# Optimization experiments

Hardware: AMD Instinct MI355X
Metric: run time of the kernel (lower is better)

The kernel has to match this reference:

```python
import jax, jax.numpy as jnp
import numpy as np

N, E, D = 50000, 800000, 64


def setup_inputs() -> dict:
    key = jax.random.key(0)
    k = jax.random.split(key, 6)
    return {
        "graph_embedding": jax.random.normal(k[0], (N, D), dtype=jnp.float32),
        "W": jax.random.normal(k[1], (D, D), dtype=jnp.float32) * (1.0 / np.sqrt(D)),
        "b": jnp.zeros((D,), dtype=jnp.float32),
        "src": jax.random.randint(k[2], (E,), 0, N),
        "dst": jax.random.randint(k[3], (E,), 0, N),
        "e_feat": jax.random.randint(k[4], (E,), 0, 8),
    }


def _gcn_both(x, src, dst, n, W=None, b=None):
    # DGL GraphConv with norm='both': D_out^{-1/2} gather-sum D_in^{-1/2}, then optional weight.
    ones = jnp.ones((src.shape[0],), x.dtype)
    out_deg = jnp.maximum(jax.ops.segment_sum(ones, src, num_segments=n), 1.0)
    in_deg = jnp.maximum(jax.ops.segment_sum(ones, dst, num_segments=n), 1.0)
    x = x * (out_deg ** -0.5)[:, None]
    agg = jax.ops.segment_sum(x[src], dst, num_segments=n)  # [N, D]
    agg = agg * (in_deg ** -0.5)[:, None]
    if W is not None:
        agg = agg @ W + b
    return agg


def reference(graph_embedding, W, b, src, dst, e_feat):
    n = graph_embedding.shape[0]
    # dropout is identity in eval mode
    h = _gcn_both(graph_embedding, src, dst, n)       # layer 0: weight=False
    h = _gcn_both(h, src, dst, n, W, b)               # layer 1: with weight + bias
    # message: ft + sum of masked copies; all ft0/ft2/ft4/ft6 == ft, so per-edge scale
    e = e_feat.reshape(-1, 1).astype(jnp.float32)     # [E, 1], mirrors e_feat.reshape(-1,1).float()
    coef = (1.0 + (e == 0.0) + (e == 2.0) + (e == 4.0) + (e == 6.0)).astype(h.dtype)
    msg = h[src] * coef                               # [E, D] edge gather + scale
    return jax.ops.segment_sum(msg, dst, num_segments=n)  # scatter-sum to dst
```

## Files before the change

### kernel.cpp

```cpp
#include <hip/hip_runtime.h>

#define DD 64
#define CHUNK_A 4096

__global__ __launch_bounds__(256) void k_pre(const int* __restrict__ src,
                                             const int* __restrict__ dst,
                                             int* __restrict__ M,
                                             int* __restrict__ cout_, int E, int PB) {
    int t = threadIdx.x;
    int bid = blockIdx.x;
    if (bid < PB) {
        __shared__ int hist[256];
        hist[t] = 0;
        __syncthreads();
        int base = bid * CHUNK_A;
#pragma unroll
        for (int k = 0; k < CHUNK_A / 256; ++k) {
            int e = base + t + (k << 8);
            if (e < E) atomicAdd(&hist[dst[e] >> 8], 1);
        }
        __syncthreads();
        M[bid * 256 + t] = hist[t];
    } else {
        int e = (bid - PB) * 256 + t;
        if (e < E) atomicAdd(&cout_[src[e]], 1);
    }
}

__global__ __launch_bounds__(256) void k_binscan(int* __restrict__ M,
                                                 int* __restrict__ binBase,
                                                 int* __restrict__ rstart,
                                                 const int* __restrict__ cout_,
                                                 float* __restrict__ oinv,
                                                 int PB, int n, int E) {
    int t = threadIdx.x;
    if (blockIdx.x == 0) {
        int tot = 0;
        for (int p = 0; p < PB; ++p) tot += M[p * 256 + t];
        int lane = t & 63, w = t >> 6;
        int inc = tot;
        for (int o = 1; o < 64; o <<= 1) {
            int u = __shfl_up(inc, o);
            if (lane >= o) inc += u;
        }
        __shared__ int wtot[4];
        if (lane == 63) wtot[w] = inc;
        __syncthreads();
        int woff = 0;
        for (int i = 0; i < w; ++i) woff += wtot[i];
        int base = woff + inc - tot;
        binBase[t] = base;
        if (t == 255) { binBase[256] = base + tot; rstart[n] = E; }
        int run = base;
#pragma unroll 4
        for (int p = 0; p < PB; ++p) {
            int v = M[p * 256 + t];
            M[p * 256 + t] = run;
            run += v;
        }
    } else {
        int i = (blockIdx.x - 1) * 256 + t;
        if (i < n) oinv[i] = rsqrtf((float)max(cout_[i], 1));
    }
}

__global__ __launch_bounds__(256) void k_scatterA(const int* __restrict__ src,
                                                  const int* __restrict__ dst,
                                                  const int* __restrict__ ef,
                                                  const int* __restrict__ M,
                                                  int* __restrict__ bucketA, int E) {
    __shared__ int cur[256];
    int t = threadIdx.x;
    int p = blockIdx.x;
    cur[t] = M[p * 256 + t];
    __syncthreads();
    int base = p * CHUNK_A;
#pragma unroll
    for (int k = 0; k < CHUNK_A / 256; ++k) {
        int e = base + t + (k << 8);
        if (e < E) {
            int d = dst[e];
            int pos = atomicAdd(&cur[d >> 8], 1);
            bucketA[pos] = src[e] | ((ef[e] & 1) << 17) | ((d & 255) << 18);
        }
    }
}

__global__ __launch_bounds__(256) void k_bucket(const int* __restrict__ bucketA,
                                                const int* __restrict__ binBase,
                                                int* __restrict__ rstart,
                                                float* __restrict__ iinv,
                                                int* __restrict__ edges, int n) {
    __shared__ int cnt[256];
    __shared__ int off[256];
    __shared__ int wtot[4];
    int t = threadIdx.x;
    int b = blockIdx.x;
    int s0 = binBase[b], s1 = binBase[b + 1];
    cnt[t] = 0;
    __syncthreads();
    for (int i = s0 + t; i < s1; i += 256)
        atomicAdd(&cnt[(bucketA[i] >> 18) & 255], 1);
    __syncthreads();
    int c = cnt[t];
    int lane = t & 63, w = t >> 6;
    int inc = c;
    for (int o = 1; o < 64; o <<= 1) {
        int u = __shfl_up(inc, o);
        if (lane >= o) inc += u;
    }
    if (lane == 63) wtot[w] = inc;
    __syncthreads();
    int woff = 0;
    for (int i = 0; i < w; ++i) woff += wtot[i];
    int excl = woff + inc - c;
    int v = b * 256 + t;
    if (v < n) {
        rstart[v] = s0 + excl;
        iinv[v] = rsqrtf((float)max(c, 1));
    }
    off[t] = excl;
    __syncthreads();
    for (int i = s0 + t; i < s1; i += 256) {
        int r = bucketA[i];
        int cc = (r >> 18) & 255;
        int pos = atomicAdd(&off[cc], 1);
        edges[s0 + pos] = (r & 0x1FFFF) | (int)(((unsigned)((r >> 17) & 1)) << 31);
    }
}

template <int MODE>
__global__ __launch_bounds__(256) void k_gather(const float* __restrict__ x,
                                                const int* __restrict__ edges,
                                                const int* __restrict__ row_start,
                                                const float* __restrict__ oinv,
                                                const float* __restrict__ iinv,
                                                float* __restrict__ y, int n) {
    int wave = (blockIdx.x * 256 + threadIdx.x) >> 6;
    if (wave >= n) return;
    int lane = threadIdx.x & 63;
    int sub = lane >> 4;
    int q = lane & 15;
    int s0 = row_start[wave], s1 = row_start[wave + 1];
    float ax = 0.f, ay = 0.f, az = 0.f, aw = 0.f;
    for (int i = s0 + sub; i < s1; i += 4) {
        int rec = edges[i];
        int s = rec & 0x7fffffff;
        const float4 v = *(const float4*)(x + (size_t)s * DD + q * 4);
        float sc = 1.0f;
        if (MODE == 0) sc = oinv[s];
        if (MODE == 2) sc = (rec < 0) ? 1.0f : 2.0f;
        ax = fmaf(v.x, sc, ax);
        ay = fmaf(v.y, sc, ay);
        az = fmaf(v.z, sc, az);
        aw = fmaf(v.w, sc, aw);
    }
    ax += __shfl_xor(ax, 16); ay += __shfl_xor(ay, 16);
    az += __shfl_xor(az, 16); aw += __shfl_xor(aw, 16);
    ax += __shfl_xor(ax, 32); ay += __shfl_xor(ay, 32);
    az += __shfl_xor(az, 32); aw += __shfl_xor(aw, 32);
    if (sub == 0) {
        float post = 1.0f;
        if (MODE == 0) post = iinv[wave] * oinv[wave];
        float4 o = make_float4(ax * post, ay * post, az * post, aw * post);
        *(float4*)(y + (size_t)wave * DD + q * 4) = o;
    }
}

__global__ __launch_bounds__(256) void k_gather_gemm(const float* __restrict__ x,
                                                     const int* __restrict__ edges,
                                                     const int* __restrict__ row_start,
                                                     const float* __restrict__ iinv,
                                                     const float* __restrict__ W,
                                                     const float* __restrict__ b,
                                                     float* __restrict__ h1, int n) {
    __shared__ float Wl[64 * 64];
    __shared__ float bl[64];
    __shared__ float wrow[4][64];
    int tid = threadIdx.x;
    const float4* W4 = (const float4*)W;
    float4* Wl4 = (float4*)Wl;
#pragma unroll
    for (int k = 0; k < 4; ++k) Wl4[tid + k * 256] = W4[tid + k * 256];
    if (tid < 64) bl[tid] = b[tid];

    int wave = (blockIdx.x * 256 + tid) >> 6;
    int lane = tid & 63;
    int sub = lane >> 4;
    int q = lane & 15;
    bool valid = wave < n;
    float ax = 0.f, ay = 0.f, az = 0.f, aw = 0.f;
    if (valid) {
        int s0 = row_start[wave], s1 = row_start[wave + 1];
        for (int i = s0 + sub; i < s1; i += 4) {
            int s = edges[i] & 0x7fffffff;
            const float4 v = *(const float4*)(x + (size_t)s * DD + q * 4);
            ax += v.x; ay += v.y; az += v.z; aw += v.w;
        }
    }
    ax += __shfl_xor(ax, 16); ay += __shfl_xor(ay, 16);
    az += __shfl_xor(az, 16); aw += __shfl_xor(aw, 16);
    ax += __shfl_xor(ax, 32); ay += __shfl_xor(ay, 32);
    az += __shfl_xor(az, 32); aw += __shfl_xor(aw, 32);
    __syncthreads();
    int wid = tid >> 6;
    if (valid && sub == 0) {
        float post = iinv[wave];
        *(float4*)&wrow[wid][q * 4] =
            make_float4(ax * post, ay * post, az * post, aw * post);
    }
    __syncthreads();
    if (valid) {
        float acc = bl[lane];
#pragma unroll
        for (int k = 0; k < 64; ++k) acc = fmaf(wrow[wid][k], Wl[k * 64 + lane], acc);
        h1[(size_t)wave * DD + lane] = acc;
    }
}

extern "C" void kernel_launch(void* const* d_in, const int* in_sizes, int n_in,
                              void* d_out, int out_size, void* d_ws, size_t ws_size,
                              hipStream_t stream) {
    const float* x   = (const float*)d_in[0];
    const float* W   = (const float*)d_in[1];
    const float* b   = (const float*)d_in[2];
    const int*   src = (const int*)d_in[3];
    const int*   dst = (const int*)d_in[4];
    const int*   ef  = (const int*)d_in[5];
    float* out = (float*)d_out;

    const int n = in_sizes[0] / DD;
    const int E = in_sizes[3];

    const int PB = (E + CHUNK_A - 1) / CHUNK_A;
    const int NB = (n + 255) >> 8;
    const int HB = (E + 255) / 256;
    const int SB = (n + 255) / 256;

    char* ws = (char*)d_ws;
    size_t np = ((size_t)n + 255) & ~(size_t)255;
    int*   cout_  = (int*)ws;   ws += np * 4;
    float* oinv   = (float*)ws; ws += np * 4;
    float* iinv   = (float*)ws; ws += np * 4;
    int*   rstart = (int*)ws;   ws += (np + 256) * 4;
    int*   binBase= (int*)ws;   ws += 260 * 4;
    int*   M      = (int*)ws;   ws += (size_t)PB * 256 * 4;
    int*   bucketA= (int*)ws;   ws += (size_t)E * 4;
    int*   edges  = (int*)ws;   ws += (size_t)E * 4;
    size_t fbytes = (size_t)n * DD * sizeof(float);
    float* h0  = (float*)ws;    ws += fbytes;
    float* agg = (float*)ws;    ws += fbytes;

    hipMemsetAsync(cout_, 0, np * 4, stream);

    k_pre<<<PB + HB, 256, 0, stream>>>(src, dst, M, cout_, E, PB);
    k_binscan<<<1 + SB, 256, 0, stream>>>(M, binBase, rstart, cout_, oinv, PB, n, E);
    k_scatterA<<<PB, 256, 0, stream>>>(src, dst, ef, M, bucketA, E);
    k_bucket<<<NB, 256, 0, stream>>>(bucketA, binBase, rstart, iinv, edges, n);

    int gblocks = (n + 3) / 4;
    k_gather<0><<<gblocks, 256, 0, stream>>>(x, edges, rstart, oinv, iinv, h0, n);
    k_gather_gemm<<<gblocks, 256, 0, stream>>>(h0, edges, rstart, iinv, W, b, agg, n);
    k_gather<2><<<gblocks, 256, 0, stream>>>(agg, edges, rstart, oinv, iinv, out, n);
}
```

Before: 293.8 us.

## Compute out-degrees via binned histogram instead of global atomics; unroll gathers by two

Out-degree counting moves from per-edge global atomics (plus a memset) to the same two-level shared-memory bin histogram used for in-degrees. It adds a byte-sized src bucket array and extra bins in the prep, scatter and bucket kernels. The gather loops are also unrolled to process two edges per iteration, giving more memory-level parallelism. The cost is extra passes over src and extra scatter traffic in preprocessing.

```diff
diff --git a/kernel.cpp b/kernel.cpp
--- a/kernel.cpp
+++ b/kernel.cpp
@@ -2,65 +2,63 @@
 
 #define DD 64
 #define CHUNK_A 4096
+#define SRC_MASK 0x1FFFF
 
 __global__ __launch_bounds__(256) void k_pre(const int* __restrict__ src,
                                              const int* __restrict__ dst,
                                              int* __restrict__ M,
-                                             int* __restrict__ cout_, int E, int PB) {
+                                             int* __restrict__ Msrc, int E) {
+    __shared__ int hd[256], hs[256];
     int t = threadIdx.x;
     int bid = blockIdx.x;
-    if (bid < PB) {
-        __shared__ int hist[256];
-        hist[t] = 0;
-        __syncthreads();
-        int base = bid * CHUNK_A;
+    hd[t] = 0; hs[t] = 0;
+    __syncthreads();
+    int base = bid * CHUNK_A;
 #pragma unroll
-        for (int k = 0; k < CHUNK_A / 256; ++k) {
-            int e = base + t + (k << 8);
-            if (e < E) atomicAdd(&hist[dst[e] >> 8], 1);
-        }
-        __syncthreads();
-        M[bid * 256 + t] = hist[t];
-    } else {
-        int e = (bid - PB) * 256 + t;
-        if (e < E) atomicAdd(&cout_[src[e]], 1);
-    }
+    for (int k = 0; k < CHUNK_A / 256; ++k) {
+        int e = base + t + (k << 8);
+        if (e < E) {
+            atomicAdd(&hd[dst[e] >> 8], 1);
+            atomicAdd(&hs[src[e] >> 8], 1);
+        }
+    }
+    __syncthreads();
+    M[bid * 256 + t] = hd[t];
+    Msrc[bid * 256 + t] = hs[t];
 }
 
 __global__ __launch_bounds__(256) void k_binscan(int* __restrict__ M,
+                                                 int* __restrict__ Msrc,
                                                  int* __restrict__ binBase,
+                                                 int* __restrict__ binBaseS,
                                                  int* __restrict__ rstart,
-                                                 const int* __restrict__ cout_,
-                                                 float* __restrict__ oinv,
                                                  int PB, int n, int E) {
     int t = threadIdx.x;
-    if (blockIdx.x == 0) {
-        int tot = 0;
-        for (int p = 0; p < PB; ++p) tot += M[p * 256 + t];
-        int lane = t & 63, w = t >> 6;
-        int inc = tot;
-        for (int o = 1; o < 64; o <<= 1) {
-            int u = __shfl_up(inc, o);
-            if (lane >= o) inc += u;
-        }
-        __shared__ int wtot[4];
-        if (lane == 63) wtot[w] = inc;
-        __syncthreads();
-        int woff = 0;
-        for (int i = 0; i < w; ++i) woff += wtot[i];
-        int base = woff + inc - tot;
-        binBase[t] = base;
-        if (t == 255) { binBase[256] = base + tot; rstart[n] = E; }
-        int run = base;
+    int* Mx = (blockIdx.x == 0) ? M : Msrc;
+    int* bb = (blockIdx.x == 0) ? binBase : binBaseS;
+    int tot = 0;
+    for (int p = 0; p < PB; ++p) tot += Mx[p * 256 + t];
+    int lane = t & 63, w = t >> 6;
+    int inc = tot;
+    for (int o = 1; o < 64; o <<= 1) {
+        int u = __shfl_up(inc, o);
+        if (lane >= o) inc += u;
+    }
+    __shared__ int wtot[4];
+    if (lane == 63) wtot[w] = inc;
+    __syncthreads();
+    int woff = 0;
+    for (int i = 0; i < w; ++i) woff += wtot[i];
+    int base = woff + inc - tot;
+    bb[t] = base;
+    if (t == 255) bb[256] = base + tot;
+    if (blockIdx.x == 0 && t == 0) rstart[n] = E;
+    int run = base;
 #pragma unroll 4
-        for (int p = 0; p < PB; ++p) {
-            int v = M[p * 256 + t];
-            M[p * 256 + t] = run;
-            run += v;
-        }
-    } else {
-        int i = (blockIdx.x - 1) * 256 + t;
-        if (i < n) oinv[i] = rsqrtf((float)max(cout_[i], 1));
+    for (int p = 0; p < PB; ++p) {
+        int v = Mx[p * 256 + t];
+        Mx[p * 256 + t] = run;
+        run += v;
     }
 }
 
@@ -68,64 +66,85 @@
                                                   const int* __restrict__ dst,
                                                   const int* __restrict__ ef,
                                                   const int* __restrict__ M,
-                                                  int* __restrict__ bucketA, int E) {
-    __shared__ int cur[256];
+                                                  const int* __restrict__ Msrc,
+                                                  int* __restrict__ bucketA,
+                                                  unsigned char* __restrict__ bucketS,
+                                                  int E) {
+    __shared__ int curD[256], curS[256];
     int t = threadIdx.x;
     int p = blockIdx.x;
-    cur[t] = M[p * 256 + t];
+    curD[t] = M[p * 256 + t];
+    curS[t] = Msrc[p * 256 + t];
     __syncthreads();
     int base = p * CHUNK_A;
 #pragma unroll
     for (int k = 0; k < CHUNK_A / 256; ++k) {
         int e = base + t + (k << 8);
         if (e < E) {
-            int d = dst[e];
-            int pos = atomicAdd(&cur[d >> 8], 1);
-            bucketA[pos] = src[e] | ((ef[e] & 1) << 17) | ((d & 255) << 18);
+            int s = src[e], d = dst[e];
+            int posD = atomicAdd(&curD[d >> 8], 1);
+            bucketA[posD] = s | ((ef[e] & 1) << 17) | ((d & 255) << 18);
+            int posS = atomicAdd(&curS[s >> 8], 1);
+            bucketS[posS] = (unsigned char)(s & 255);
         }
     }
 }
 
 __global__ __launch_bounds__(256) void k_bucket(const int* __restrict__ bucketA,
+                                                const unsigned char* __restrict__ bucketS,
                                                 const int* __restrict__ binBase,
+                                                const int* __restrict__ binBaseS,
                                                 int* __restrict__ rstart,
                                                 float* __restrict__ iinv,
-                                                int* __restrict__ edges, int n) {
+                                                float* __restrict__ oinv,
+                                                int* __restrict__ edges, int n, int NB) {
     __shared__ int cnt[256];
     __shared__ int off[256];
     __shared__ int wtot[4];
     int t = threadIdx.x;
     int b = blockIdx.x;
-    int s0 = binBase[b], s1 = binBase[b + 1];
-    cnt[t] = 0;
-    __syncthreads();
-    for (int i = s0 + t; i < s1; i += 256)
-        atomicAdd(&cnt[(bucketA[i] >> 18) & 255], 1);
-    __syncthreads();
-    int c = cnt[t];
-    int lane = t & 63, w = t >> 6;
-    int inc = c;
-    for (int o = 1; o < 64; o <<= 1) {
-        int u = __shfl_up(inc, o);
-        if (lane >= o) inc += u;
-    }
-    if (lane == 63) wtot[w] = inc;
-    __syncthreads();
-    int woff = 0;
-    for (int i = 0; i < w; ++i) woff += wtot[i];
-    int excl = woff + inc - c;
-    int v = b * 256 + t;
-    if (v < n) {
-        rstart[v] = s0 + excl;
-        iinv[v] = rsqrtf((float)max(c, 1));
-    }
-    off[t] = excl;
-    __syncthreads();
-    for (int i = s0 + t; i < s1; i += 256) {
-        int r = bucketA[i];
-        int cc = (r >> 18) & 255;
-        int pos = atomicAdd(&off[cc], 1);
-        edges[s0 + pos] = (r & 0x1FFFF) | (int)(((unsigned)((r >> 17) & 1)) << 31);
+    if (b < NB) {
+        int s0 = binBase[b], s1 = binBase[b + 1];
+        cnt[t] = 0;
+        __syncthreads();
+        for (int i = s0 + t; i < s1; i += 256)
+            atomicAdd(&cnt[(bucketA[i] >> 18) & 255], 1);
+        __syncthreads();
+        int c = cnt[t];
+        int lane = t & 63, w = t >> 6;
+        int inc = c;
+        for (int o = 1; o < 64; o <<= 1) {
+            int u = __shfl_up(inc, o);
+            if (lane >= o) inc += u;
+        }
+        if (lane == 63) wtot[w] = inc;
+        __syncthreads();
+        int woff = 0;
+        for (int i = 0; i < w; ++i) woff += wtot[i];
+        int excl = woff + inc - c;
+        int v = b * 256 + t;
+        if (v < n) {
+            rstart[v] = s0 + excl;
+            iinv[v] = rsqrtf((float)max(c, 1));
+        }
+        off[t] = excl;
+        __syncthreads();
+        for (int i = s0 + t; i < s1; i += 256) {
+            int r = bucketA[i];
+            int cc = (r >> 18) & 255;
+            int pos = atomicAdd(&off[cc], 1);
+            edges[s0 + pos] = (r & SRC_MASK) | (int)(((unsigned)((r >> 17) & 1)) << 31);
+        }
+    } else {
+        int bs = b - NB;
+        int s0 = binBaseS[bs], s1 = binBaseS[bs + 1];
+        cnt[t] = 0;
+        __syncthreads();
+        for (int i = s0 + t; i < s1; i += 256)
+            atomicAdd(&cnt[(int)bucketS[i]], 1);
+        __syncthreads();
+        int v = bs * 256 + t;
+        if (v < n) oinv[v] = rsqrtf((float)max(cnt[t], 1));
     }
 }
 
@@ -143,17 +162,29 @@
     int q = lane & 15;
     int s0 = row_start[wave], s1 = row_start[wave + 1];
     float ax = 0.f, ay = 0.f, az = 0.f, aw = 0.f;
-    for (int i = s0 + sub; i < s1; i += 4) {
-        int rec = edges[i];
-        int s = rec & 0x7fffffff;
-        const float4 v = *(const float4*)(x + (size_t)s * DD + q * 4);
-        float sc = 1.0f;
-        if (MODE == 0) sc = oinv[s];
-        if (MODE == 2) sc = (rec < 0) ? 1.0f : 2.0f;
-        ax = fmaf(v.x, sc, ax);
-        ay = fmaf(v.y, sc, ay);
-        az = fmaf(v.z, sc, az);
-        aw = fmaf(v.w, sc, aw);
+    int i = s0 + sub;
+    for (; i + 4 < s1; i += 8) {
+        int r0 = edges[i], r1 = edges[i + 4];
+        int sa = r0 & SRC_MASK, sb = r1 & SRC_MASK;
+        const float4 v0 = *(const float4*)(x + (size_t)sa * DD + q * 4);
+        const float4 v1 = *(const float4*)(x + (size_t)sb * DD + q * 4);
+        float c0 = 1.0f, c1 = 1.0f;
+        if (MODE == 0) { c0 = oinv[sa]; c1 = oinv[sb]; }
+        if (MODE == 2) { c0 = (r0 < 0) ? 1.0f : 2.0f; c1 = (r1 < 0) ? 1.0f : 2.0f; }
+        ax = fmaf(v0.x, c0, ax); ay = fmaf(v0.y, c0, ay);
+        az = fmaf(v0.z, c0, az); aw = fmaf(v0.w, c0, aw);
+        ax = fmaf(v1.x, c1, ax); ay = fmaf(v1.y, c1, ay);
+        az = fmaf(v1.z, c1, az); aw = fmaf(v1.w, c1, aw);
+    }
+    if (i < s1) {
+        int r0 = edges[i];
+        int sa = r0 & SRC_MASK;
+        const float4 v0 = *(const float4*)(x + (size_t)sa * DD + q * 4);
+        float c0 = 1.0f;
+        if (MODE == 0) c0 = oinv[sa];
+        if (MODE == 2) c0 = (r0 < 0) ? 1.0f : 2.0f;
+        ax = fmaf(v0.x, c0, ax); ay = fmaf(v0.y, c0, ay);
+        az = fmaf(v0.z, c0, az); aw = fmaf(v0.w, c0, aw);
     }
     ax += __shfl_xor(ax, 16); ay += __shfl_xor(ay, 16);
     az += __shfl_xor(az, 16); aw += __shfl_xor(aw, 16);
@@ -192,10 +223,18 @@
     float ax = 0.f, ay = 0.f, az = 0.f, aw = 0.f;
     if (valid) {
         int s0 = row_start[wave], s1 = row_start[wave + 1];
-        for (int i = s0 + sub; i < s1; i += 4) {
-            int s = edges[i] & 0x7fffffff;
-            const float4 v = *(const float4*)(x + (size_t)s * DD + q * 4);
-            ax += v.x; ay += v.y; az += v.z; aw += v.w;
+        int i = s0 + sub;
+        for (; i + 4 < s1; i += 8) {
+            int sa = edges[i] & SRC_MASK, sb = edges[i + 4] & SRC_MASK;
+            const float4 v0 = *(const float4*)(x + (size_t)sa * DD + q * 4);
+            const float4 v1 = *(const float4*)(x + (size_t)sb * DD + q * 4);
+            ax += v0.x; ay += v0.y; az += v0.z; aw += v0.w;
+            ax += v1.x; ay += v1.y; az += v1.z; aw += v1.w;
+        }
+        if (i < s1) {
+            int sa = edges[i] & SRC_MASK;
+            const float4 v0 = *(const float4*)(x + (size_t)sa * DD + q * 4);
+            ax += v0.x; ay += v0.y; az += v0.z; aw += v0.w;
         }
     }
     ax += __shfl_xor(ax, 16); ay += __shfl_xor(ay, 16);
@@ -234,29 +273,28 @@
 
     const int PB = (E + CHUNK_A - 1) / CHUNK_A;
     const int NB = (n + 255) >> 8;
-    const int HB = (E + 255) / 256;
-    const int SB = (n + 255) / 256;
 
     char* ws = (char*)d_ws;
     size_t np = ((size_t)n + 255) & ~(size_t)255;
-    int*   cout_  = (int*)ws;   ws += np * 4;
-    float* oinv   = (float*)ws; ws += np * 4;
-    float* iinv   = (float*)ws; ws += np * 4;
-    int*   rstart = (int*)ws;   ws += (np + 256) * 4;
-    int*   binBase= (int*)ws;   ws += 260 * 4;
-    int*   M      = (int*)ws;   ws += (size_t)PB * 256 * 4;
-    int*   bucketA= (int*)ws;   ws += (size_t)E * 4;
-    int*   edges  = (int*)ws;   ws += (size_t)E * 4;
+    float* oinv    = (float*)ws; ws += np * 4;
+    float* iinv    = (float*)ws; ws += np * 4;
+    int*   rstart  = (int*)ws;   ws += (np + 256) * 4;
+    int*   binBase = (int*)ws;   ws += 260 * 4;
+    int*   binBaseS= (int*)ws;   ws += 260 * 4;
+    int*   M       = (int*)ws;   ws += (size_t)PB * 256 * 4;
+    int*   Msrc    = (int*)ws;   ws += (size_t)PB * 256 * 4;
+    int*   bucketA = (int*)ws;   ws += (size_t)E * 4;
+    unsigned char* bucketS = (unsigned char*)ws; ws += ((size_t)E + 255) & ~(size_t)255;
+    int*   edges   = (int*)ws;   ws += (size_t)E * 4;
     size_t fbytes = (size_t)n * DD * sizeof(float);
     float* h0  = (float*)ws;    ws += fbytes;
     float* agg = (float*)ws;    ws += fbytes;
 
-    hipMemsetAsync(cout_, 0, np * 4, stream);
-
-    k_pre<<<PB + HB, 256, 0, stream>>>(src, dst, M, cout_, E, PB);
-    k_binscan<<<1 + SB, 256, 0, stream>>>(M, binBase, rstart, cout_, oinv, PB, n, E);
-    k_scatterA<<<PB, 256, 0, stream>>>(src, dst, ef, M, bucketA, E);
-    k_bucket<<<NB, 256, 0, stream>>>(bucketA, binBase, rstart, iinv, edges, n);
+    k_pre<<<PB, 256, 0, stream>>>(src, dst, M, Msrc, E);
+    k_binscan<<<2, 256, 0, stream>>>(M, Msrc, binBase, binBaseS, rstart, PB, n, E);
+    k_scatterA<<<PB, 256, 0, stream>>>(src, dst, ef, M, Msrc, bucketA, bucketS, E);
+    k_bucket<<<2 * NB, 256, 0, stream>>>(bucketA, bucketS, binBase, binBaseS,
+                                         rstart, iinv, oinv, edges, n, NB);
 
     int gblocks = (n + 3) / 4;
     k_gather<0><<<gblocks, 256, 0, stream>>>(x, edges, rstart, oinv, iinv, h0, n);
```

Result: faster. 256.3 us (-12.8%).
